# Performance work log

Measured on AMD Instinct MI355X. Metric: run time of the kernel, lower is better.

## Reference

```python
import jax, jax.numpy as jnp
import numpy as np

B, C_IN, C_OUT, H, W = 16, 64, 64, 192, 192
K_DY, KS, STRIDE, PAD = 4, 3, 1, 1
TEMP = 30.0
HID = int(C_IN * 0.25) + 1  # 17, matches hidden_channels rule for in_channels != 3
GROUPS = 8
EPS = 1e-5
NEG_SLOPE = 0.01


def setup_inputs() -> dict:
    key = jax.random.key(0)
    ks = jax.random.split(key, 6)
    return {
        "x": jax.random.normal(ks[0], (B, C_IN, H, W), jnp.float32),
        "attn_w1": jax.random.normal(ks[1], (HID, C_IN), jnp.float32) * 0.1,   # 1x1 conv, no bias
        "attn_w2": jax.random.normal(ks[2], (K_DY, HID), jnp.float32) * 0.1,   # 1x1 conv
        "attn_b2": jnp.zeros((K_DY,), jnp.float32),
        "weights": jax.random.normal(ks[3], (K_DY, C_OUT, C_IN, KS, KS), jnp.float32),
        "gn_gamma": jnp.ones((C_OUT,), jnp.float32),
        "gn_beta": jnp.zeros((C_OUT,), jnp.float32),
    }


def reference(x, attn_w1, attn_w2, attn_b2, weights, gn_gamma, gn_beta):
    b = x.shape[0]
    # SE-style attention over the dynamic-filter bank
    pooled = x.mean(axis=(2, 3))                       # (b, c_in) global avg pool
    h = jax.nn.relu(pooled @ attn_w1.T)                # (b, hid)
    scores = h @ attn_w2.T + attn_b2                   # (b, K)
    attn = jax.nn.softmax(scores / TEMP, axis=1)       # (b, K)
    # Per-sample synthesized filters
    filters = jnp.einsum('bk,koihw->boihw', attn, weights)   # (b, out_c, in_c, kh, kw)
    filters = filters.reshape(b * C_OUT, C_IN, KS, KS)
    # Grouped conv: groups = batch, each sample convolved with its own filter
    xg = x.reshape(1, b * C_IN, H, W)
    y = jax.lax.conv_general_dilated(
        xg, filters,
        window_strides=(STRIDE, STRIDE),
        padding=[(PAD, PAD), (PAD, PAD)],
        dimension_numbers=('NCHW', 'OIHW', 'NCHW'),
        feature_group_count=b,
    )
    y = y.reshape(b, C_OUT, y.shape[2], y.shape[3])
    # GroupNorm(8 groups) + LeakyReLU
    yg = y.reshape(b, GROUPS, C_OUT // GROUPS, y.shape[2], y.shape[3])
    mean = yg.mean(axis=(2, 3, 4), keepdims=True)
    var = yg.var(axis=(2, 3, 4), keepdims=True)
    yn = ((yg - mean) * jax.lax.rsqrt(var + EPS)).reshape(y.shape)
    yn = yn * gn_gamma[None, :, None, None] + gn_beta[None, :, None, None]
    return jnp.where(yn >= 0, yn, NEG_SLOPE * yn)
```

## Files before the change

kernel.cpp:

```cpp
#include <hip/hip_runtime.h>

typedef unsigned short u16;
typedef unsigned int u32;
typedef _Float16 f16;
typedef __attribute__((ext_vector_type(8))) f16 v8h;
typedef __attribute__((ext_vector_type(4))) f16 v4h;
typedef __attribute__((ext_vector_type(16))) float v16f;

#define BN 16
#define CHN 64
#define HH 192
#define WW 192
#define HWSZ 36864
#define KDY 4
#define HIDN 17
#define NG 8
#define TEMP_ 30.0f
#define EPSV 1e-5f
#define NSLOPE 0.01f
#define NTILE 144

#define TR 8
#define TC 32
#define HR 10
#define HC 34
#define PSTR 34
#define NCHUNK (HR * HC * 8)

__device__ float g_pp[BN * NTILE * CHN];
__device__ float g_attn[BN * KDY];
__device__ float g_stats[BN * NG * 2];
__device__ __align__(16) f16 g_filt[BN * 9 * CHN * CHN];
__device__ __align__(16) f16 g_xh[(size_t)BN * HWSZ * CHN];
__device__ __align__(16) f16 g_yh[(size_t)BN * CHN * HWSZ];

__global__ void __launch_bounds__(256) trans_pool_kernel(const float* __restrict__ x) {
    __shared__ u32 ts[256 * 34];
    const int b = blockIdx.y, tile = blockIdx.x;
    const int t = threadIdx.x;
    const int p0 = tile * 256;
    const float* xb = x + (size_t)b * CHN * HWSZ + p0;
    #pragma unroll 4
    for (int cp = 0; cp < 32; cp++) {
        float v0 = xb[(size_t)(2 * cp) * HWSZ + t];
        float v1 = xb[(size_t)(2 * cp + 1) * HWSZ + t];
        u32 pk = (u32)__builtin_bit_cast(u16, (f16)v0)
               | ((u32)__builtin_bit_cast(u16, (f16)v1) << 16);
        ts[t * 34 + cp] = pk;
    }
    __syncthreads();
    f16* dp = g_xh + ((size_t)b * HWSZ + p0 + t) * CHN;
    const u32* src = ts + t * 34;
    #pragma unroll
    for (int i = 0; i < 8; i++) {
        uint2 a = *(const uint2*)(src + 4 * i);
        uint2 c = *(const uint2*)(src + 4 * i + 2);
        ((uint4*)dp)[i] = make_uint4(a.x, a.y, c.x, c.y);
    }
    const int cp = t & 31, seg = t >> 5;
    float s0 = 0.f, s1 = 0.f;
    for (int p = 0; p < 32; p++) {
        u32 pk = ts[(seg * 32 + p) * 34 + cp];
        s0 += (float)__builtin_bit_cast(f16, (u16)(pk & 0xffffu));
        s1 += (float)__builtin_bit_cast(f16, (u16)(pk >> 16));
    }
    s0 += __shfl_down(s0, 32);
    s1 += __shfl_down(s1, 32);
    __syncthreads();
    float* ps = (float*)ts;
    const int lane = t & 63, w = t >> 6;
    if (lane < 32) { ps[(w * 32 + lane) * 2] = s0; ps[(w * 32 + lane) * 2 + 1] = s1; }
    __syncthreads();
    if (t < 32) {
        float a0 = ps[t * 2] + ps[(32 + t) * 2] + ps[(64 + t) * 2] + ps[(96 + t) * 2];
        float a1 = ps[t * 2 + 1] + ps[(32 + t) * 2 + 1]
                 + ps[(64 + t) * 2 + 1] + ps[(96 + t) * 2 + 1];
        float* gp = g_pp + ((size_t)b * NTILE + tile) * CHN;
        gp[2 * t] = a0; gp[2 * t + 1] = a1;
    }
}

__global__ void __launch_bounds__(256) attn_kernel(const float* __restrict__ w1,
                                                   const float* __restrict__ w2,
                                                   const float* __restrict__ b2) {
    __shared__ float red[256];
    __shared__ float pr[CHN];
    __shared__ float hs[HIDN];
    const int b = blockIdx.x, t = threadIdx.x;
    if (t < NG * 2) g_stats[b * NG * 2 + t] = 0.f;
    const int c = t & 63, part = t >> 6;
    const float* gp = g_pp + (size_t)b * NTILE * CHN + c;
    float s = 0.f;
    #pragma unroll 4
    for (int i = part * 36; i < part * 36 + 36; i++) s += gp[i * CHN];
    red[t] = s;
    __syncthreads();
    if (t < CHN)
        pr[t] = (red[t] + red[t + 64] + red[t + 128] + red[t + 192]) * (1.0f / HWSZ);
    __syncthreads();
    if (t < HIDN) {
        float a = 0.f;
        for (int cc = 0; cc < CHN; cc++) a += w1[t * CHN + cc] * pr[cc];
        hs[t] = fmaxf(a, 0.f);
    }
    __syncthreads();
    if (t == 0) {
        float scv[KDY]; float m = -3e38f;
        #pragma unroll
        for (int k = 0; k < KDY; k++) {
            float sc = b2[k];
            for (int h = 0; h < HIDN; h++) sc += w2[k * HIDN + h] * hs[h];
            sc *= (1.0f / TEMP_);
            scv[k] = sc; m = fmaxf(m, sc);
        }
        float den = 0.f;
        #pragma unroll
        for (int k = 0; k < KDY; k++) { scv[k] = __expf(scv[k] - m); den += scv[k]; }
        float rd = 1.f / den;
        #pragma unroll
        for (int k = 0; k < KDY; k++) g_attn[b * KDY + k] = scv[k] * rd;
    }
}

__global__ void filt_kernel(const float* __restrict__ wts) {
    __shared__ float at[BN * KDY];
    if (threadIdx.x < BN * KDY) at[threadIdx.x] = g_attn[threadIdx.x];
    __syncthreads();
    int t = blockIdx.x * 256 + threadIdx.x;
    int tap = t / 4096;
    int co = (t >> 6) & 63;
    int ci = t & 63;
    float w0 = wts[((0 * CHN + co) * CHN + ci) * 9 + tap];
    float w1 = wts[((1 * CHN + co) * CHN + ci) * 9 + tap];
    float w2 = wts[((2 * CHN + co) * CHN + ci) * 9 + tap];
    float w3 = wts[((3 * CHN + co) * CHN + ci) * 9 + tap];
    #pragma unroll
    for (int b = 0; b < BN; b++) {
        float v = at[b * 4] * w0 + at[b * 4 + 1] * w1
                + at[b * 4 + 2] * w2 + at[b * 4 + 3] * w3;
        g_filt[((b * 9 + tap) * CHN + co) * CHN + ci] = (f16)v;
    }
}

__global__ void __launch_bounds__(256, 3) conv_kernel() {
    __shared__ __align__(16) u32 xs[HR * HC * PSTR];
    __shared__ float gsum[NG], gsq[NG];
    const int bid = blockIdx.x;
    const int swz = (bid & 7) * 288 + (bid >> 3);
    const int b = swz / 144;
    const int rem = swz - b * 144;
    const int r0 = (rem / 6) * TR, c0 = (rem % 6) * TC;
    const int tid = threadIdx.x;
    const int w = tid >> 6, lane = tid & 63;
    const int n = lane & 31, hi = lane >> 5;
    if (tid < NG) { gsum[tid] = 0.f; gsq[tid] = 0.f; }

    const f16* xhb = g_xh + (size_t)b * HWSZ * CHN;
    uint4 rv[11];
    #pragma unroll
    for (int i = 0; i < 11; i++) {
        int l = tid + i * 256;
        int pix = l >> 3, part = l & 7;
        int hr = pix / HC, hc = pix - hr * HC;
        int gr = r0 - 1 + hr, gc = c0 - 1 + hc;
        bool ok = (l < NCHUNK) && ((unsigned)gr < HH) && ((unsigned)gc < WW);
        size_t off = ok ? ((size_t)(gr * WW + gc) * CHN + part * 8) : 0;
        rv[i] = *(const uint4*)(xhb + off);
    }
    #pragma unroll
    for (int i = 0; i < 11; i++) {
        int l = tid + i * 256;
        if (l < NCHUNK) {
            int pix = l >> 3, part = l & 7;
            int hr = pix / HC, hc = pix - hr * HC;
            int gr = r0 - 1 + hr, gc = c0 - 1 + hc;
            bool ok = ((unsigned)gr < HH) && ((unsigned)gc < WW);
            uint4 v = ok ? rv[i] : make_uint4(0, 0, 0, 0);
            u32* d = xs + pix * PSTR + part * 4;
            *(uint2*)d = make_uint2(v.x, v.y);
            *(uint2*)(d + 2) = make_uint2(v.z, v.w);
        }
    }
    __syncthreads();

    const f16* xsh = (const f16*)xs;
    const f16* fb = g_filt + (size_t)b * 9 * CHN * CHN + (size_t)n * CHN + hi * 8;
    v16f acc00 = {}, acc01 = {}, acc10 = {}, acc11 = {};

    v8h A0[4], A1[4];
    #pragma unroll
    for (int kb = 0; kb < 4; kb++) {
        A0[kb] = *(const v8h*)(fb + kb * 16);
        A1[kb] = *(const v8h*)(fb + kb * 16 + 32 * CHN);
    }
    #pragma unroll
    for (int tap = 0; tap < 9; tap++) {
        v8h P0[4], P1[4];
        if (tap < 8) {
            const f16* fp = fb + (tap + 1) * (CHN * CHN);
            #pragma unroll
            for (int kb = 0; kb < 4; kb++) {
                P0[kb] = *(const v8h*)(fp + kb * 16);
                P1[kb] = *(const v8h*)(fp + kb * 16 + 32 * CHN);
            }
        }
        const int dy = tap / 3, dx = tap - 3 * (tap / 3);
        const f16* xr = xsh + ((2 * w + dy) * HC + (n + dx)) * (PSTR * 2) + hi * 8;
        #pragma unroll
        for (int kb = 0; kb < 4; kb++) {
            v4h lo0 = *(const v4h*)(xr + kb * 16);
            v4h up0 = *(const v4h*)(xr + kb * 16 + 4);
            v4h lo1 = *(const v4h*)(xr + kb * 16 + HC * PSTR * 2);
            v4h up1 = *(const v4h*)(xr + kb * 16 + 4 + HC * PSTR * 2);
            v8h b0 = __builtin_shufflevector(lo0, up0, 0, 1, 2, 3, 4, 5, 6, 7);
            v8h b1 = __builtin_shufflevector(lo1, up1, 0, 1, 2, 3, 4, 5, 6, 7);
            acc00 = __builtin_amdgcn_mfma_f32_32x32x16_f16(A0[kb], b0, acc00, 0, 0, 0);
            acc01 = __builtin_amdgcn_mfma_f32_32x32x16_f16(A0[kb], b1, acc01, 0, 0, 0);
            acc10 = __builtin_amdgcn_mfma_f32_32x32x16_f16(A1[kb], b0, acc10, 0, 0, 0);
            acc11 = __builtin_amdgcn_mfma_f32_32x32x16_f16(A1[kb], b1, acc11, 0, 0, 0);
        }
        if (tap < 8) {
            #pragma unroll
            for (int kb = 0; kb < 4; kb++) { A0[kb] = P0[kb]; A1[kb] = P1[kb]; }
        }
    }

    float sg[NG], sq[NG];
    #pragma unroll
    for (int g = 0; g < NG; g++) { sg[g] = 0.f; sq[g] = 0.f; }
    f16* yb = g_yh + (size_t)b * CHN * HWSZ + (size_t)(r0 + 2 * w) * WW + (c0 + n);
#define EPI(ACC, CH, J) { v16f a = ACC; \
    _Pragma("unroll") \
    for (int r = 0; r < 16; r++) { \
        int co = CH * 32 + (r & 3) + 8 * (r >> 2) + 4 * hi; \
        yb[(size_t)co * HWSZ + J * WW] = (f16)a[r]; \
        int g = (r >> 2) + 4 * CH; \
        sg[g] += a[r]; sq[g] += a[r] * a[r]; } }
    EPI(acc00, 0, 0) EPI(acc01, 0, 1) EPI(acc10, 1, 0) EPI(acc11, 1, 1)
#undef EPI
    #pragma unroll
    for (int g = 0; g < NG; g++) {
        float s = sg[g], q = sq[g];
        #pragma unroll
        for (int off = 32; off > 0; off >>= 1) {
            s += __shfl_down(s, off);
            q += __shfl_down(q, off);
        }
        if (lane == 0) { atomicAdd(&gsum[g], s); atomicAdd(&gsq[g], q); }
    }
    __syncthreads();
    if (tid < 2 * NG) {
        int g = tid >> 1, which = tid & 1;
        atomicAdd(&g_stats[(b * NG + g) * 2 + which], which ? gsq[g] : gsum[g]);
    }
}

__global__ void norm_kernel(float* __restrict__ out, const float* __restrict__ gamma,
                            const float* __restrict__ beta) {
    int i8 = blockIdx.x * 256 + threadIdx.x;
    int idx = i8 * 8;
    int b = idx / (CHN * HWSZ);
    int co = (idx / HWSZ) & (CHN - 1);
    int g = co >> 3;
    const float invN = 1.0f / (8.0f * HWSZ);
    float mean = g_stats[(b * NG + g) * 2 + 0] * invN;
    float var = fmaxf(g_stats[(b * NG + g) * 2 + 1] * invN - mean * mean, 0.f);
    float sc = rsqrtf(var + EPSV) * gamma[co];
    float sh = beta[co] - mean * sc;
    v8h v = *(const v8h*)(g_yh + (size_t)idx);
    float vv[8];
    #pragma unroll
    for (int t = 0; t < 8; t++) {
        float a = (float)v[t] * sc + sh;
        vv[t] = a >= 0.f ? a : NSLOPE * a;
    }
    float4* op = (float4*)out + i8 * 2;
    op[0] = make_float4(vv[0], vv[1], vv[2], vv[3]);
    op[1] = make_float4(vv[4], vv[5], vv[6], vv[7]);
}

extern "C" void kernel_launch(void* const* d_in, const int* in_sizes, int n_in,
                              void* d_out, int out_size, void* d_ws, size_t ws_size,
                              hipStream_t stream) {
    const float* x     = (const float*)d_in[0];
    const float* w1    = (const float*)d_in[1];
    const float* w2    = (const float*)d_in[2];
    const float* b2    = (const float*)d_in[3];
    const float* wts   = (const float*)d_in[4];
    const float* gamma = (const float*)d_in[5];
    const float* beta  = (const float*)d_in[6];
    float* out = (float*)d_out;

    dim3 tg(NTILE, BN);
    trans_pool_kernel<<<tg, 256, 0, stream>>>(x);
    attn_kernel<<<BN, 256, 0, stream>>>(w1, w2, b2);
    filt_kernel<<<144, 256, 0, stream>>>(wts);
    conv_kernel<<<2304, 256, 0, stream>>>();
    norm_kernel<<<BN * CHN * HWSZ / 8 / 256, 256, 0, stream>>>(out, gamma, beta);
}
```

Before: 406.7 us.

## Halve conv tile height, split warps over output channels, batch norm work per block

Result: no change. 408.8 us (+0.5%).

```diff
diff --git a/kernel.cpp b/kernel.cpp
--- a/kernel.cpp
+++ b/kernel.cpp
@@ -20,12 +20,14 @@
 #define NSLOPE 0.01f
 #define NTILE 144
 
-#define TR 8
+#define TR 4
 #define TC 32
-#define HR 10
+#define HR 6
 #define HC 34
 #define PSTR 34
+#define ROWH (HC * PSTR * 2)
 #define NCHUNK (HR * HC * 8)
+#define NBLK 4608
 
 __device__ float g_pp[BN * NTILE * CHN];
 __device__ float g_attn[BN * KDY];
@@ -142,23 +144,24 @@
     }
 }
 
-__global__ void __launch_bounds__(256, 3) conv_kernel() {
+__global__ void __launch_bounds__(256, 5) conv_kernel() {
     __shared__ __align__(16) u32 xs[HR * HC * PSTR];
     __shared__ float gsum[NG], gsq[NG];
     const int bid = blockIdx.x;
-    const int swz = (bid & 7) * 288 + (bid >> 3);
-    const int b = swz / 144;
-    const int rem = swz - b * 144;
+    const int swz = (bid & 7) * 576 + (bid >> 3);
+    const int b = swz / 288;
+    const int rem = swz - b * 288;
     const int r0 = (rem / 6) * TR, c0 = (rem % 6) * TC;
     const int tid = threadIdx.x;
     const int w = tid >> 6, lane = tid & 63;
+    const int wr = w >> 1, wc = w & 1;
     const int n = lane & 31, hi = lane >> 5;
     if (tid < NG) { gsum[tid] = 0.f; gsq[tid] = 0.f; }
 
     const f16* xhb = g_xh + (size_t)b * HWSZ * CHN;
-    uint4 rv[11];
-    #pragma unroll
-    for (int i = 0; i < 11; i++) {
+    uint4 rv[7];
+    #pragma unroll
+    for (int i = 0; i < 7; i++) {
         int l = tid + i * 256;
         int pix = l >> 3, part = l & 7;
         int hr = pix / HC, hc = pix - hr * HC;
@@ -168,7 +171,7 @@
         rv[i] = *(const uint4*)(xhb + off);
     }
     #pragma unroll
-    for (int i = 0; i < 11; i++) {
+    for (int i = 0; i < 7; i++) {
         int l = tid + i * 256;
         if (l < NCHUNK) {
             int pix = l >> 3, part = l & 7;
@@ -184,69 +187,62 @@
     __syncthreads();
 
     const f16* xsh = (const f16*)xs;
-    const f16* fb = g_filt + (size_t)b * 9 * CHN * CHN + (size_t)n * CHN + hi * 8;
-    v16f acc00 = {}, acc01 = {}, acc10 = {}, acc11 = {};
-
-    v8h A0[4], A1[4];
-    #pragma unroll
-    for (int kb = 0; kb < 4; kb++) {
-        A0[kb] = *(const v8h*)(fb + kb * 16);
-        A1[kb] = *(const v8h*)(fb + kb * 16 + 32 * CHN);
-    }
+    const f16* fb = g_filt + (size_t)b * 9 * CHN * CHN
+                  + (size_t)(wc * 32 + n) * CHN + hi * 8;
+    v16f acc0 = {}, acc1 = {};
+
+    v8h A[4];
+    #pragma unroll
+    for (int kb = 0; kb < 4; kb++) A[kb] = *(const v8h*)(fb + kb * 16);
     #pragma unroll
     for (int tap = 0; tap < 9; tap++) {
-        v8h P0[4], P1[4];
+        v8h P[4];
         if (tap < 8) {
             const f16* fp = fb + (tap + 1) * (CHN * CHN);
             #pragma unroll
-            for (int kb = 0; kb < 4; kb++) {
-                P0[kb] = *(const v8h*)(fp + kb * 16);
-                P1[kb] = *(const v8h*)(fp + kb * 16 + 32 * CHN);
-            }
+            for (int kb = 0; kb < 4; kb++) P[kb] = *(const v8h*)(fp + kb * 16);
         }
         const int dy = tap / 3, dx = tap - 3 * (tap / 3);
-        const f16* xr = xsh + ((2 * w + dy) * HC + (n + dx)) * (PSTR * 2) + hi * 8;
+        const f16* xr = xsh + ((2 * wr + dy) * HC + (n + dx)) * (PSTR * 2) + hi * 8;
+        __builtin_amdgcn_s_setprio(1);
         #pragma unroll
         for (int kb = 0; kb < 4; kb++) {
             v4h lo0 = *(const v4h*)(xr + kb * 16);
             v4h up0 = *(const v4h*)(xr + kb * 16 + 4);
-            v4h lo1 = *(const v4h*)(xr + kb * 16 + HC * PSTR * 2);
-            v4h up1 = *(const v4h*)(xr + kb * 16 + 4 + HC * PSTR * 2);
+            v4h lo1 = *(const v4h*)(xr + kb * 16 + ROWH);
+            v4h up1 = *(const v4h*)(xr + kb * 16 + 4 + ROWH);
             v8h b0 = __builtin_shufflevector(lo0, up0, 0, 1, 2, 3, 4, 5, 6, 7);
             v8h b1 = __builtin_shufflevector(lo1, up1, 0, 1, 2, 3, 4, 5, 6, 7);
-            acc00 = __builtin_amdgcn_mfma_f32_32x32x16_f16(A0[kb], b0, acc00, 0, 0, 0);
-            acc01 = __builtin_amdgcn_mfma_f32_32x32x16_f16(A0[kb], b1, acc01, 0, 0, 0);
-            acc10 = __builtin_amdgcn_mfma_f32_32x32x16_f16(A1[kb], b0, acc10, 0, 0, 0);
-            acc11 = __builtin_amdgcn_mfma_f32_32x32x16_f16(A1[kb], b1, acc11, 0, 0, 0);
-        }
+            acc0 = __builtin_amdgcn_mfma_f32_32x32x16_f16(A[kb], b0, acc0, 0, 0, 0);
+            acc1 = __builtin_amdgcn_mfma_f32_32x32x16_f16(A[kb], b1, acc1, 0, 0, 0);
+        }
+        __builtin_amdgcn_s_setprio(0);
         if (tap < 8) {
             #pragma unroll
-            for (int kb = 0; kb < 4; kb++) { A0[kb] = P0[kb]; A1[kb] = P1[kb]; }
-        }
-    }
-
-    float sg[NG], sq[NG];
-    #pragma unroll
-    for (int g = 0; g < NG; g++) { sg[g] = 0.f; sq[g] = 0.f; }
-    f16* yb = g_yh + (size_t)b * CHN * HWSZ + (size_t)(r0 + 2 * w) * WW + (c0 + n);
-#define EPI(ACC, CH, J) { v16f a = ACC; \
-    _Pragma("unroll") \
-    for (int r = 0; r < 16; r++) { \
-        int co = CH * 32 + (r & 3) + 8 * (r >> 2) + 4 * hi; \
-        yb[(size_t)co * HWSZ + J * WW] = (f16)a[r]; \
-        int g = (r >> 2) + 4 * CH; \
-        sg[g] += a[r]; sq[g] += a[r] * a[r]; } }
-    EPI(acc00, 0, 0) EPI(acc01, 0, 1) EPI(acc10, 1, 0) EPI(acc11, 1, 1)
-#undef EPI
-    #pragma unroll
-    for (int g = 0; g < NG; g++) {
-        float s = sg[g], q = sq[g];
+            for (int kb = 0; kb < 4; kb++) A[kb] = P[kb];
+        }
+    }
+
+    float sg[4] = {0.f, 0.f, 0.f, 0.f}, sq[4] = {0.f, 0.f, 0.f, 0.f};
+    f16* yb = g_yh + (size_t)b * CHN * HWSZ + (size_t)(r0 + 2 * wr) * WW + (c0 + n);
+    #pragma unroll
+    for (int r = 0; r < 16; r++) {
+        int co = wc * 32 + (r & 3) + 8 * (r >> 2) + 4 * hi;
+        float a0 = acc0[r], a1 = acc1[r];
+        yb[(size_t)co * HWSZ] = (f16)a0;
+        yb[(size_t)co * HWSZ + WW] = (f16)a1;
+        int gl = r >> 2;
+        sg[gl] += a0 + a1; sq[gl] += a0 * a0 + a1 * a1;
+    }
+    #pragma unroll
+    for (int gl = 0; gl < 4; gl++) {
+        float s = sg[gl], q = sq[gl];
         #pragma unroll
         for (int off = 32; off > 0; off >>= 1) {
             s += __shfl_down(s, off);
             q += __shfl_down(q, off);
         }
-        if (lane == 0) { atomicAdd(&gsum[g], s); atomicAdd(&gsq[g], q); }
+        if (lane == 0) { atomicAdd(&gsum[4 * wc + gl], s); atomicAdd(&gsq[4 * wc + gl], q); }
     }
     __syncthreads();
     if (tid < 2 * NG) {
@@ -255,28 +251,33 @@
     }
 }
 
-__global__ void norm_kernel(float* __restrict__ out, const float* __restrict__ gamma,
-                            const float* __restrict__ beta) {
-    int i8 = blockIdx.x * 256 + threadIdx.x;
-    int idx = i8 * 8;
-    int b = idx / (CHN * HWSZ);
-    int co = (idx / HWSZ) & (CHN - 1);
-    int g = co >> 3;
+__global__ void __launch_bounds__(256) norm_kernel(float* __restrict__ out,
+                                                   const float* __restrict__ gamma,
+                                                   const float* __restrict__ beta) {
+    const int tid = threadIdx.x;
     const float invN = 1.0f / (8.0f * HWSZ);
-    float mean = g_stats[(b * NG + g) * 2 + 0] * invN;
-    float var = fmaxf(g_stats[(b * NG + g) * 2 + 1] * invN - mean * mean, 0.f);
-    float sc = rsqrtf(var + EPSV) * gamma[co];
-    float sh = beta[co] - mean * sc;
-    v8h v = *(const v8h*)(g_yh + (size_t)idx);
-    float vv[8];
-    #pragma unroll
-    for (int t = 0; t < 8; t++) {
-        float a = (float)v[t] * sc + sh;
-        vv[t] = a >= 0.f ? a : NSLOPE * a;
-    }
-    float4* op = (float4*)out + i8 * 2;
-    op[0] = make_float4(vv[0], vv[1], vv[2], vv[3]);
-    op[1] = make_float4(vv[4], vv[5], vv[6], vv[7]);
+    #pragma unroll
+    for (int it = 0; it < 8; it++) {
+        int ch = it * 2304 + blockIdx.x;
+        int bco = ch / 18;
+        int b = bco >> 6, co = bco & 63;
+        int g = co >> 3;
+        float mean = g_stats[(b * NG + g) * 2 + 0] * invN;
+        float var = fmaxf(g_stats[(b * NG + g) * 2 + 1] * invN - mean * mean, 0.f);
+        float sc = rsqrtf(var + EPSV) * gamma[co];
+        float sh = beta[co] - mean * sc;
+        size_t base = (size_t)ch * 2048 + tid * 8;
+        v8h v = *(const v8h*)(g_yh + base);
+        float vv[8];
+        #pragma unroll
+        for (int t = 0; t < 8; t++) {
+            float a = (float)v[t] * sc + sh;
+            vv[t] = a >= 0.f ? a : NSLOPE * a;
+        }
+        float4* op = (float4*)(out + base);
+        op[0] = make_float4(vv[0], vv[1], vv[2], vv[3]);
+        op[1] = make_float4(vv[4], vv[5], vv[6], vv[7]);
+    }
 }
 
 extern "C" void kernel_launch(void* const* d_in, const int* in_sizes, int n_in,
@@ -295,6 +296,6 @@
     trans_pool_kernel<<<tg, 256, 0, stream>>>(x);
     attn_kernel<<<BN, 256, 0, stream>>>(w1, w2, b2);
     filt_kernel<<<144, 256, 0, stream>>>(wts);
-    conv_kernel<<<2304, 256, 0, stream>>>();
-    norm_kernel<<<BN * CHN * HWSZ / 8 / 256, 256, 0, stream>>>(out, gamma, beta);
-}
+    conv_kernel<<<NBLK, 256, 0, stream>>>();
+    norm_kernel<<<2304, 256, 0, stream>>>(out, gamma, beta);
+}
```
